# Kernel tuning notes

Measured on AMD Instinct MI355X. Metric: run time of the kernel, lower is better.

The kernel has to match this reference:

```python
import jax, jax.numpy as jnp
import numpy as np

NEG_SLOPE = 0.2
EPS = 1e-16

N_NODES = 50000
N_EDGES = 800000
IN_DIM = 64
HEADS = 4
HEAD_DIM = 64


def setup_inputs() -> dict:
    key = jax.random.key(0)
    k1, k2, k3, k4, k5 = jax.random.split(key, 5)
    x = jax.random.normal(k1, (N_NODES, IN_DIM), dtype=jnp.float32)
    edge_index = jax.random.randint(k2, (2, N_EDGES), 0, N_NODES, dtype=jnp.int64)
    W = jax.random.normal(k3, (IN_DIM, HEADS * HEAD_DIM), dtype=jnp.float32) * (1.0 / np.sqrt(IN_DIM))
    att_src = jax.random.normal(k4, (HEADS, HEAD_DIM), dtype=jnp.float32) * 0.1
    att_dst = jax.random.normal(k5, (HEADS, HEAD_DIM), dtype=jnp.float32) * 0.1
    bias = jnp.zeros((HEADS * HEAD_DIM,), dtype=jnp.float32)
    return {"x": x, "edge_index": edge_index, "W": W,
            "att_src": att_src, "att_dst": att_dst, "bias": bias}


def reference(x, edge_index, W, att_src, att_dst, bias):
    N = x.shape[0]
    H, D = att_src.shape
    # add self-loops (PyG default add_self_loops=True)
    loop = jnp.arange(N, dtype=edge_index.dtype)
    src = jnp.concatenate([edge_index[0], loop])  # message source j
    dst = jnp.concatenate([edge_index[1], loop])  # message target i

    h = (x @ W).reshape(N, H, D)                 # [N,H,D] per-head projection
    a_src = jnp.einsum('nhd,hd->nh', h, att_src)  # [N,H]
    a_dst = jnp.einsum('nhd,hd->nh', h, att_dst)  # [N,H]

    score = jax.nn.leaky_relu(a_src[src] + a_dst[dst], NEG_SLOPE)  # [E,H]
    # segment softmax over edges grouped by destination node
    m = jax.ops.segment_max(score, dst, num_segments=N)            # [N,H]
    m = jnp.where(jnp.isfinite(m), m, 0.0)
    e = jnp.exp(score - m[dst])                                    # [E,H]
    denom = jax.ops.segment_sum(e, dst, num_segments=N)            # [N,H]
    alpha = e / (denom[dst] + EPS)                                 # [E,H]

    msgs = h[src] * alpha[:, :, None]                              # [E,H,D]
    out = jax.ops.segment_sum(msgs, dst, num_segments=N)           # [N,H,D]
    return out.reshape(N, H * D) + bias
```

## Files before the change

### kernel.cpp

```cpp
#include <hip/hip_runtime.h>

#define N_NODES 50000
#define N_EDGES 800000
#define E_TOT   850000
#define HD      256
#define MAXDEG  64
#define NEG_SLOPE 0.2f
#define EPS 1e-16f

#define NB     98
#define BSHIFT 9
#define CAP    10240
#define ABLK   392
#define EPB    2304

typedef __attribute__((ext_vector_type(8))) short short8;
typedef __attribute__((ext_vector_type(4))) float f32x4;

__device__ __forceinline__ unsigned short f2bf(float f) {
    union { float f; unsigned int i; } c; c.f = f;
    unsigned int r = 0x7fffu + ((c.i >> 16) & 1u);
    return (unsigned short)((c.i + r) >> 16);
}
__device__ __forceinline__ float bf2f(unsigned short u) {
    union { unsigned int i; float f; } c; c.i = ((unsigned int)u) << 16;
    return c.f;
}
__device__ __forceinline__ short8 pack8(float4 a, float4 b) {
    short8 r;
    r[0] = (short)f2bf(a.x); r[1] = (short)f2bf(a.y);
    r[2] = (short)f2bf(a.z); r[3] = (short)f2bf(a.w);
    r[4] = (short)f2bf(b.x); r[5] = (short)f2bf(b.y);
    r[6] = (short)f2bf(b.z); r[7] = (short)f2bf(b.w);
    return r;
}
__device__ __forceinline__ float lrelu_exp(float v) {
    v = (v < 0.f) ? v * NEG_SLOPE : v;
    return __expf(v);
}

__global__ __launch_bounds__(256) void prep_kernel(
        const float* __restrict__ W, const float* __restrict__ att_src,
        const float* __restrict__ att_dst, float* __restrict__ ws, float* __restrict__ wd,
        int* __restrict__ gcnt) {
    const int t = threadIdx.x, head = t >> 6, k = t & 63;
    if (t < 128) gcnt[t] = 0;
    const float* wrow = W + k * 256 + head * 64;
    const float* as = att_src + head * 64;
    const float* adv = att_dst + head * 64;
    float s = 0.f, d = 0.f;
#pragma unroll 8
    for (int j = 0; j < 64; ++j) { s += wrow[j] * as[j]; d += wrow[j] * adv[j]; }
    ws[k * 4 + head] = s;
    wd[k * 4 + head] = d;
}

__global__ __launch_bounds__(256) void bin_logit_kernel(
        const float* __restrict__ x,
        const float4* __restrict__ ws4, const float4* __restrict__ wd4,
        const int* __restrict__ eidx,
        int* __restrict__ gcnt, unsigned int* __restrict__ arena,
        float4* __restrict__ a_src4, float4* __restrict__ a_dst4,
        unsigned short* __restrict__ xb) {
    __shared__ int hist[4][NB];
    __shared__ int abase[4][NB];
    const int t = threadIdx.x;
    const int w = t >> 6;
    const int e0 = blockIdx.x * EPB;
    for (int i = t; i < 4 * NB; i += 256) ((int*)hist)[i] = 0;
    __syncthreads();

#pragma unroll
    for (int k = 0; k < EPB / 256; ++k) {
        const int g = e0 + k * 256 + t;
        if (g < E_TOT) {
            const int d = (g < N_EDGES) ? eidx[N_EDGES + g] : g - N_EDGES;
            atomicAdd(&hist[w][d >> BSHIFT], 1);
        }
    }
    __syncthreads();
    if (t < NB) {
        const int c0 = hist[0][t], c1 = hist[1][t], c2 = hist[2][t], c3 = hist[3][t];
        const int tot = c0 + c1 + c2 + c3;
        const int base = tot ? atomicAdd(&gcnt[t], tot) : 0;
        abase[0][t] = base;
        abase[1][t] = base + c0;
        abase[2][t] = base + c0 + c1;
        abase[3][t] = base + c0 + c1 + c2;
        hist[0][t] = 0; hist[1][t] = 0; hist[2][t] = 0; hist[3][t] = 0;
    }
    __syncthreads();

#pragma unroll
    for (int k = 0; k < EPB / 256; ++k) {
        const int g = e0 + k * 256 + t;
        if (g < E_TOT) {
            int s, d;
            if (g < N_EDGES) { s = eidx[g]; d = eidx[N_EDGES + g]; }
            else             { s = d = g - N_EDGES; }
            const int b = d >> BSHIFT;
            const int pos = abase[w][b] + atomicAdd(&hist[w][b], 1);
            if (pos < CAP)
                arena[b * CAP + pos] =
                    (unsigned int)s | ((unsigned int)(d & 511) << 16);
        }
    }

    const int g = blockIdx.x * 256 + t;
    if (g < N_NODES) {
        const float4* xr = (const float4*)(x + (size_t)g * 64);
        float4 vs = {0.f, 0.f, 0.f, 0.f};
        float4 vd = {0.f, 0.f, 0.f, 0.f};
#pragma unroll 4
        for (int kk = 0; kk < 16; kk += 2) {
            float4 xv0 = xr[kk];
            float4 xv1 = xr[kk + 1];
            *(short8*)&xb[(size_t)g * 64 + kk * 4] = pack8(xv0, xv1);
#pragma unroll
            for (int j = 0; j < 8; ++j) {
                const float4 xv = (j < 4) ? xv0 : xv1;
                const int jj = j & 3;
                const float xj = jj == 0 ? xv.x : jj == 1 ? xv.y : jj == 2 ? xv.z : xv.w;
                const float4 w1 = ws4[(kk + (j >> 2)) * 4 + jj];
                const float4 w2 = wd4[(kk + (j >> 2)) * 4 + jj];
                vs.x += xj * w1.x; vs.y += xj * w1.y; vs.z += xj * w1.z; vs.w += xj * w1.w;
                vd.x += xj * w2.x; vd.y += xj * w2.y; vd.z += xj * w2.z; vd.w += xj * w2.w;
            }
        }
        a_src4[g] = vs;
        a_dst4[g] = vd;
    }
}

__global__ __launch_bounds__(1024) void ell_build_kernel(
        const int* __restrict__ gcnt, const unsigned int* __restrict__ arena,
        int* __restrict__ cnt, unsigned short* __restrict__ slotu) {
    __shared__ int lcnt[512];
    const int t = threadIdx.x;
    const int b = blockIdx.x;
    if (t < 512) lcnt[t] = 0;
    __syncthreads();
    int m = gcnt[b]; if (m > CAP) m = CAP;
    const int n0 = b << BSHIFT;
    const unsigned int* ap = arena + (size_t)b * CAP;
    const uint4* ap4 = (const uint4*)ap;
    const int m4 = m >> 2;
    for (int i = t; i < m4; i += 1024) {
        const uint4 p4 = ap4[i];
#pragma unroll
        for (int j = 0; j < 4; ++j) {
            const unsigned int p = j == 0 ? p4.x : j == 1 ? p4.y : j == 2 ? p4.z : p4.w;
            const int dl = p >> 16;
            const int s  = p & 0xFFFFu;
            const int pos = atomicAdd(&lcnt[dl], 1);
            if (pos < MAXDEG) slotu[(size_t)(n0 + dl) * MAXDEG + pos] = (unsigned short)s;
        }
    }
    for (int i = (m4 << 2) + t; i < m; i += 1024) {
        const unsigned int p = ap[i];
        const int dl = p >> 16;
        const int s  = p & 0xFFFFu;
        const int pos = atomicAdd(&lcnt[dl], 1);
        if (pos < MAXDEG) slotu[(size_t)(n0 + dl) * MAXDEG + pos] = (unsigned short)s;
    }
    __syncthreads();
    if (t < 512) {
        const int n = n0 + t;
        if (n < N_NODES) cnt[n] = lcnt[t];
    }
}

__global__ __launch_bounds__(256) void aggregate_x_kernel(
        const int* __restrict__ cnt, const unsigned short* __restrict__ slotu,
        const float4* __restrict__ a_src4, const float4* __restrict__ a_dst4,
        const unsigned short* __restrict__ xb, unsigned short* __restrict__ yb) {
    __shared__ int    lsrc[4][64];
    __shared__ float4 lscs[4][64];
    const int w    = threadIdx.x >> 6;
    const int lane = threadIdx.x & 63;
    const int node = blockIdx.x * 4 + w;
    int deg = cnt[node];
    if (deg > MAXDEG) deg = MAXDEG;
    const size_t base = (size_t)node * MAXDEG;
    const float4 ad = a_dst4[node];

    int s = (lane < deg) ? (int)slotu[base + lane] : 0;
    float4 A = a_src4[s];
    float4 sc;
    if (lane < deg) {
        sc.x = lrelu_exp(A.x + ad.x); sc.y = lrelu_exp(A.y + ad.y);
        sc.z = lrelu_exp(A.z + ad.z); sc.w = lrelu_exp(A.w + ad.w);
    } else {
        sc = (float4){0.f, 0.f, 0.f, 0.f};
    }
    lsrc[w][lane] = s;
    lscs[w][lane] = sc;

    float4 ds = sc;
#pragma unroll
    for (int m = 1; m < 64; m <<= 1) {
        ds.x += __shfl_xor(ds.x, m, 64); ds.y += __shfl_xor(ds.y, m, 64);
        ds.z += __shfl_xor(ds.z, m, 64); ds.w += __shfl_xor(ds.w, m, 64);
    }
    float4 inv;
    inv.x = 1.f / (ds.x + EPS); inv.y = 1.f / (ds.y + EPS);
    inv.z = 1.f / (ds.z + EPS); inv.w = 1.f / (ds.w + EPS);

    const int g  = lane >> 4;
    const int dg = lane & 15;
    float acc[4][4];
#pragma unroll
    for (int h = 0; h < 4; ++h)
#pragma unroll
        for (int j = 0; j < 4; ++j) acc[h][j] = 0.f;

    const int nit = (deg + 3) >> 2;
    for (int it = 0; it < nit; ++it) {
        const int e = it * 4 + g;
        const int se = lsrc[w][e];
        const float4 ce = lscs[w][e];
        const ushort4 xv = *(const ushort4*)&xb[(size_t)se * 64 + dg * 4];
        const float x0 = bf2f(xv.x), x1 = bf2f(xv.y), x2 = bf2f(xv.z), x3 = bf2f(xv.w);
        acc[0][0] += x0 * ce.x; acc[0][1] += x1 * ce.x; acc[0][2] += x2 * ce.x; acc[0][3] += x3 * ce.x;
        acc[1][0] += x0 * ce.y; acc[1][1] += x1 * ce.y; acc[1][2] += x2 * ce.y; acc[1][3] += x3 * ce.y;
        acc[2][0] += x0 * ce.z; acc[2][1] += x1 * ce.z; acc[2][2] += x2 * ce.z; acc[2][3] += x3 * ce.z;
        acc[3][0] += x0 * ce.w; acc[3][1] += x1 * ce.w; acc[3][2] += x2 * ce.w; acc[3][3] += x3 * ce.w;
    }

#pragma unroll
    for (int h = 0; h < 4; ++h)
#pragma unroll
        for (int j = 0; j < 4; ++j) {
            acc[h][j] += __shfl_xor(acc[h][j], 16, 64);
            acc[h][j] += __shfl_xor(acc[h][j], 32, 64);
        }

    const float iv = g == 0 ? inv.x : g == 1 ? inv.y : g == 2 ? inv.z : inv.w;
    const float o0 = (g == 0 ? acc[0][0] : g == 1 ? acc[1][0] : g == 2 ? acc[2][0] : acc[3][0]) * iv;
    const float o1 = (g == 0 ? acc[0][1] : g == 1 ? acc[1][1] : g == 2 ? acc[2][1] : acc[3][1]) * iv;
    const float o2 = (g == 0 ? acc[0][2] : g == 1 ? acc[1][2] : g == 2 ? acc[2][2] : acc[3][2]) * iv;
    const float o3 = (g == 0 ? acc[0][3] : g == 1 ? acc[1][3] : g == 2 ? acc[2][3] : acc[3][3]) * iv;
    ushort4 ov;
    ov.x = f2bf(o0); ov.y = f2bf(o1); ov.z = f2bf(o2); ov.w = f2bf(o3);
    *(ushort4*)&yb[(size_t)node * 256 + g * 64 + dg * 4] = ov;
}

__global__ __launch_bounds__(256) void gemm_out_kernel(
        const unsigned short* __restrict__ yb, const float* __restrict__ W,
        const float* __restrict__ bias, float* __restrict__ out) {
    __shared__ __align__(16) unsigned short Wt[256 * 64];
    const int t = threadIdx.x;
    {
        const int c = t;
        for (int kg = 0; kg < 8; ++kg) {
            float4 lo, hi;
            lo.x = W[(kg * 8 + 0) * 256 + c]; lo.y = W[(kg * 8 + 1) * 256 + c];
            lo.z = W[(kg * 8 + 2) * 256 + c]; lo.w = W[(kg * 8 + 3) * 256 + c];
            hi.x = W[(kg * 8 + 4) * 256 + c]; hi.y = W[(kg * 8 + 5) * 256 + c];
            hi.z = W[(kg * 8 + 6) * 256 + c]; hi.w = W[(kg * 8 + 7) * 256 + c];
            *(short8*)&Wt[c * 64 + ((kg ^ (c & 7)) << 3)] = pack8(lo, hi);
        }
    }
    __syncthreads();

    const int wave = t >> 6, lane = t & 63;
    const int q = lane >> 4, mloc = lane & 15;
    const int rowbase = blockIdx.x * 64 + wave * 16;
    int arow = rowbase + mloc;
    if (arow > N_NODES - 1) arow = N_NODES - 1;

    short8 a0[4], a1[4];
#pragma unroll
    for (int h = 0; h < 4; ++h) {
        const unsigned short* yr = yb + (size_t)arow * 256 + h * 64;
        a0[h] = *(const short8*)&yr[q * 8];
        a1[h] = *(const short8*)&yr[32 + q * 8];
    }

    f32x4 acc[16];
#pragma unroll
    for (int n = 0; n < 16; ++n) acc[n] = (f32x4){0.f, 0.f, 0.f, 0.f};
#pragma unroll
    for (int n = 0; n < 16; ++n) {
        const int c = n * 16 + mloc;
        const int h = n >> 2;
        const unsigned short* rowp = &Wt[c * 64];
        short8 b0 = *(const short8*)&rowp[((q    ) ^ (c & 7)) << 3];
        short8 b1 = *(const short8*)&rowp[((4 + q) ^ (c & 7)) << 3];
        acc[n] = __builtin_amdgcn_mfma_f32_16x16x32_bf16(a0[h], b0, acc[n], 0, 0, 0);
        acc[n] = __builtin_amdgcn_mfma_f32_16x16x32_bf16(a1[h], b1, acc[n], 0, 0, 0);
    }

    float bv[16];
#pragma unroll
    for (int n = 0; n < 16; ++n) bv[n] = bias[n * 16 + mloc];

    const int orow = rowbase + q * 4;
#pragma unroll
    for (int r = 0; r < 4; ++r) {
        if (orow + r < N_NODES) {
            float* op = out + (size_t)(orow + r) * 256 + mloc;
#pragma unroll
            for (int n = 0; n < 16; ++n) op[n * 16] = acc[n][r] + bv[n];
        }
    }
}

extern "C" void kernel_launch(void* const* d_in, const int* in_sizes, int n_in,
                              void* d_out, int out_size, void* d_ws, size_t ws_size,
                              hipStream_t stream) {
    const float* x       = (const float*)d_in[0];
    const int*   eidx    = (const int*)  d_in[1];
    const float* W       = (const float*)d_in[2];
    const float* att_src = (const float*)d_in[3];
    const float* att_dst = (const float*)d_in[4];
    const float* bias    = (const float*)d_in[5];
    float* out = (float*)d_out;

    unsigned short* yb = (unsigned short*)d_ws;
    float* a_src = (float*)(yb + (size_t)N_NODES * HD);
    float* a_dst = a_src + N_NODES * 4;
    float* ws    = a_dst + N_NODES * 4;
    float* wd    = ws + 256;
    int*   cnt   = (int*)(wd + 256);
    int*   gcnt  = cnt + N_NODES;
    unsigned int*   arena = (unsigned int*)(gcnt + 128);
    unsigned short* slotu = (unsigned short*)(arena + NB * CAP);
    unsigned short* xb    = slotu + (size_t)N_NODES * MAXDEG;

    prep_kernel<<<1, 256, 0, stream>>>(W, att_src, att_dst, ws, wd, gcnt);
    bin_logit_kernel<<<ABLK, 256, 0, stream>>>(
        x, (const float4*)ws, (const float4*)wd, eidx, gcnt, arena,
        (float4*)a_src, (float4*)a_dst, xb);
    ell_build_kernel<<<NB, 1024, 0, stream>>>(gcnt, arena, cnt, slotu);
    aggregate_x_kernel<<<N_NODES / 4, 256, 0, stream>>>(
        cnt, slotu, (const float4*)a_src, (const float4*)a_dst, xb, yb);
    gemm_out_kernel<<<(N_NODES + 63) / 64, 256, 0, stream>>>(yb, W, bias, out);
}
```

Before: 168.9 us.

## Use finer destination buckets, non-temporal loads, and software-pipelined gather loop

Bucketing now uses 392 bins of 128 nodes instead of 98 bins of 512, so the ELL build runs with 392 blocks of 256 threads. That spreads the work over more CUs and shrinks the shared-memory counters. The arena and slot reads now use non-temporal loads. The aggregation loop handles two edges per group per iteration and prefetches the next iteration's source features, which increases memory-level parallelism but uses more registers. The per-bin capacity of 2944 leaves less headroom for skewed degree distributions.

```diff
diff --git a/kernel.cpp b/kernel.cpp
--- a/kernel.cpp
+++ b/kernel.cpp
@@ -8,14 +8,15 @@
 #define NEG_SLOPE 0.2f
 #define EPS 1e-16f
 
-#define NB     98
-#define BSHIFT 9
-#define CAP    10240
+#define NB     392
+#define BSHIFT 7
+#define CAP    2944
 #define ABLK   392
 #define EPB    2304
 
 typedef __attribute__((ext_vector_type(8))) short short8;
 typedef __attribute__((ext_vector_type(4))) float f32x4;
+typedef __attribute__((ext_vector_type(4))) unsigned int uint4v;
 
 __device__ __forceinline__ unsigned short f2bf(float f) {
     union { float f; unsigned int i; } c; c.f = f;
@@ -44,7 +45,7 @@
         const float* __restrict__ att_dst, float* __restrict__ ws, float* __restrict__ wd,
         int* __restrict__ gcnt) {
     const int t = threadIdx.x, head = t >> 6, k = t & 63;
-    if (t < 128) gcnt[t] = 0;
+    gcnt[t] = 0; gcnt[t + 256] = 0;
     const float* wrow = W + k * 256 + head * 64;
     const float* as = att_src + head * 64;
     const float* adv = att_dst + head * 64;
@@ -79,15 +80,15 @@
         }
     }
     __syncthreads();
-    if (t < NB) {
-        const int c0 = hist[0][t], c1 = hist[1][t], c2 = hist[2][t], c3 = hist[3][t];
+    for (int i = t; i < NB; i += 256) {
+        const int c0 = hist[0][i], c1 = hist[1][i], c2 = hist[2][i], c3 = hist[3][i];
         const int tot = c0 + c1 + c2 + c3;
-        const int base = tot ? atomicAdd(&gcnt[t], tot) : 0;
-        abase[0][t] = base;
-        abase[1][t] = base + c0;
-        abase[2][t] = base + c0 + c1;
-        abase[3][t] = base + c0 + c1 + c2;
-        hist[0][t] = 0; hist[1][t] = 0; hist[2][t] = 0; hist[3][t] = 0;
+        const int base = tot ? atomicAdd(&gcnt[i], tot) : 0;
+        abase[0][i] = base;
+        abase[1][i] = base + c0;
+        abase[2][i] = base + c0 + c1;
+        abase[3][i] = base + c0 + c1 + c2;
+        hist[0][i] = 0; hist[1][i] = 0; hist[2][i] = 0; hist[3][i] = 0;
     }
     __syncthreads();
 
@@ -102,7 +103,7 @@
             const int pos = abase[w][b] + atomicAdd(&hist[w][b], 1);
             if (pos < CAP)
                 arena[b * CAP + pos] =
-                    (unsigned int)s | ((unsigned int)(d & 511) << 16);
+                    (unsigned int)s | ((unsigned int)(d & 127) << 16);
         }
     }
 
@@ -132,31 +133,31 @@
     }
 }
 
-__global__ __launch_bounds__(1024) void ell_build_kernel(
+__global__ __launch_bounds__(256) void ell_build_kernel(
         const int* __restrict__ gcnt, const unsigned int* __restrict__ arena,
         int* __restrict__ cnt, unsigned short* __restrict__ slotu) {
-    __shared__ int lcnt[512];
+    __shared__ int lcnt[128];
     const int t = threadIdx.x;
     const int b = blockIdx.x;
-    if (t < 512) lcnt[t] = 0;
+    if (t < 128) lcnt[t] = 0;
     __syncthreads();
     int m = gcnt[b]; if (m > CAP) m = CAP;
     const int n0 = b << BSHIFT;
     const unsigned int* ap = arena + (size_t)b * CAP;
-    const uint4* ap4 = (const uint4*)ap;
+    const uint4v* ap4 = (const uint4v*)ap;
     const int m4 = m >> 2;
-    for (int i = t; i < m4; i += 1024) {
-        const uint4 p4 = ap4[i];
+    for (int i = t; i < m4; i += 256) {
+        const uint4v p4 = __builtin_nontemporal_load(ap4 + i);
 #pragma unroll
         for (int j = 0; j < 4; ++j) {
-            const unsigned int p = j == 0 ? p4.x : j == 1 ? p4.y : j == 2 ? p4.z : p4.w;
+            const unsigned int p = p4[j];
             const int dl = p >> 16;
             const int s  = p & 0xFFFFu;
             const int pos = atomicAdd(&lcnt[dl], 1);
             if (pos < MAXDEG) slotu[(size_t)(n0 + dl) * MAXDEG + pos] = (unsigned short)s;
         }
     }
-    for (int i = (m4 << 2) + t; i < m; i += 1024) {
+    for (int i = (m4 << 2) + t; i < m; i += 256) {
         const unsigned int p = ap[i];
         const int dl = p >> 16;
         const int s  = p & 0xFFFFu;
@@ -164,7 +165,7 @@
         if (pos < MAXDEG) slotu[(size_t)(n0 + dl) * MAXDEG + pos] = (unsigned short)s;
     }
     __syncthreads();
-    if (t < 512) {
+    if (t < 128) {
         const int n = n0 + t;
         if (n < N_NODES) cnt[n] = lcnt[t];
     }
@@ -184,7 +185,7 @@
     const size_t base = (size_t)node * MAXDEG;
     const float4 ad = a_dst4[node];
 
-    int s = (lane < deg) ? (int)slotu[base + lane] : 0;
+    int s = (lane < deg) ? (int)__builtin_nontemporal_load(&slotu[base + lane]) : 0;
     float4 A = a_src4[s];
     float4 sc;
     if (lane < deg) {
@@ -214,17 +215,32 @@
 #pragma unroll
         for (int j = 0; j < 4; ++j) acc[h][j] = 0.f;
 
-    const int nit = (deg + 3) >> 2;
+    const int nit = (deg + 7) >> 3;
+    float4 cA = lscs[w][g], cB = lscs[w][g + 4];
+    int sA = lsrc[w][g], sB = lsrc[w][g + 4];
+    ushort4 xA = *(const ushort4*)&xb[(size_t)sA * 64 + dg * 4];
+    ushort4 xB = *(const ushort4*)&xb[(size_t)sB * 64 + dg * 4];
     for (int it = 0; it < nit; ++it) {
-        const int e = it * 4 + g;
-        const int se = lsrc[w][e];
-        const float4 ce = lscs[w][e];
-        const ushort4 xv = *(const ushort4*)&xb[(size_t)se * 64 + dg * 4];
-        const float x0 = bf2f(xv.x), x1 = bf2f(xv.y), x2 = bf2f(xv.z), x3 = bf2f(xv.w);
-        acc[0][0] += x0 * ce.x; acc[0][1] += x1 * ce.x; acc[0][2] += x2 * ce.x; acc[0][3] += x3 * ce.x;
-        acc[1][0] += x0 * ce.y; acc[1][1] += x1 * ce.y; acc[1][2] += x2 * ce.y; acc[1][3] += x3 * ce.y;
-        acc[2][0] += x0 * ce.z; acc[2][1] += x1 * ce.z; acc[2][2] += x2 * ce.z; acc[2][3] += x3 * ce.z;
-        acc[3][0] += x0 * ce.w; acc[3][1] += x1 * ce.w; acc[3][2] += x2 * ce.w; acc[3][3] += x3 * ce.w;
+        ushort4 xnA = xA, xnB = xB;
+        float4 cnA = cA, cnB = cB;
+        if (it + 1 < nit) {
+            const int en = (it + 1) * 8 + g;
+            const int snA = lsrc[w][en], snB = lsrc[w][en + 4];
+            cnA = lscs[w][en]; cnB = lscs[w][en + 4];
+            xnA = *(const ushort4*)&xb[(size_t)snA * 64 + dg * 4];
+            xnB = *(const ushort4*)&xb[(size_t)snB * 64 + dg * 4];
+        }
+        const float a0 = bf2f(xA.x), a1 = bf2f(xA.y), a2 = bf2f(xA.z), a3 = bf2f(xA.w);
+        acc[0][0] += a0 * cA.x; acc[0][1] += a1 * cA.x; acc[0][2] += a2 * cA.x; acc[0][3] += a3 * cA.x;
+        acc[1][0] += a0 * cA.y; acc[1][1] += a1 * cA.y; acc[1][2] += a2 * cA.y; acc[1][3] += a3 * cA.y;
+        acc[2][0] += a0 * cA.z; acc[2][1] += a1 * cA.z; acc[2][2] += a2 * cA.z; acc[2][3] += a3 * cA.z;
+        acc[3][0] += a0 * cA.w; acc[3][1] += a1 * cA.w; acc[3][2] += a2 * cA.w; acc[3][3] += a3 * cA.w;
+        const float b0 = bf2f(xB.x), b1 = bf2f(xB.y), b2 = bf2f(xB.z), b3 = bf2f(xB.w);
+        acc[0][0] += b0 * cB.x; acc[0][1] += b1 * cB.x; acc[0][2] += b2 * cB.x; acc[0][3] += b3 * cB.x;
+        acc[1][0] += b0 * cB.y; acc[1][1] += b1 * cB.y; acc[1][2] += b2 * cB.y; acc[1][3] += b3 * cB.y;
+        acc[2][0] += b0 * cB.z; acc[2][1] += b1 * cB.z; acc[2][2] += b2 * cB.z; acc[2][3] += b3 * cB.z;
+        acc[3][0] += b0 * cB.w; acc[3][1] += b1 * cB.w; acc[3][2] += b2 * cB.w; acc[3][3] += b3 * cB.w;
+        xA = xnA; xB = xnB; cA = cnA; cB = cnB;
     }
 
 #pragma unroll
@@ -324,7 +340,7 @@
     float* wd    = ws + 256;
     int*   cnt   = (int*)(wd + 256);
     int*   gcnt  = cnt + N_NODES;
-    unsigned int*   arena = (unsigned int*)(gcnt + 128);
+    unsigned int*   arena = (unsigned int*)(gcnt + 512);
     unsigned short* slotu = (unsigned short*)(arena + NB * CAP);
     unsigned short* xb    = slotu + (size_t)N_NODES * MAXDEG;
 
@@ -332,7 +348,7 @@
     bin_logit_kernel<<<ABLK, 256, 0, stream>>>(
         x, (const float4*)ws, (const float4*)wd, eidx, gcnt, arena,
         (float4*)a_src, (float4*)a_dst, xb);
-    ell_build_kernel<<<NB, 1024, 0, stream>>>(gcnt, arena, cnt, slotu);
+    ell_build_kernel<<<NB, 256, 0, stream>>>(gcnt, arena, cnt, slotu);
     aggregate_x_kernel<<<N_NODES / 4, 256, 0, stream>>>(
         cnt, slotu, (const float4*)a_src, (const float4*)a_dst, xb, yb);
     gemm_out_kernel<<<(N_NODES + 63) / 64, 256, 0, stream>>>(yb, W, bias, out);
```

New measurement: 174.0 us. +3.0%, slower.
